# Kernel optimization log

Hardware: AMD Instinct MI355X
Metric: run time of the kernel (lower is better)

Reference implementation:

```python
import jax, jax.numpy as jnp
import numpy as np
from jax import lax

PATCH = 11          # patch_size
DIL = 2             # dilation_patch
PAD = (PATCH // 2) * DIL  # 10
EPS = 1e-5


def setup_inputs() -> dict:
    key = jax.random.key(0)
    k0, k1, kw, kb, kg, kbe = jax.random.split(key, 6)
    B, C, H, W = 8, 128, 192, 192
    x0 = jax.random.normal(k0, (B, C, H, W), dtype=jnp.float32)
    x1 = jax.random.normal(k1, (B, C, H, W), dtype=jnp.float32)
    # Conv2d(121, 8, k=3, s=1, p=1) params + BatchNorm2d(8) affine params
    conv_w = jax.random.normal(kw, (8, 121, 3, 3), dtype=jnp.float32) * 0.05
    conv_b = jax.random.normal(kb, (8,), dtype=jnp.float32) * 0.05
    gamma = jnp.ones((8,), dtype=jnp.float32)
    beta = jnp.zeros((8,), dtype=jnp.float32)
    return {"x0": x0, "x1": x1, "conv_w": conv_w, "conv_b": conv_b,
            "gamma": gamma, "beta": beta}


def _correlation(x0, x1):
    """spatial_correlation_sample(kernel=1, patch=11, stride=1, pad=0, dil_patch=2).
    out[b, pi*11+pj, i, j] = sum_c x0[b,c,i,j] * x1[b,c, i+(pi-5)*2, j+(pj-5)*2]
    (zero-padded outside)."""
    x1p = jnp.pad(x1, ((0, 0), (0, 0), (PAD, PAD), (PAD, PAD)))
    slices = []
    for pi in range(PATCH):       # static 11x11 displacement grid
        for pj in range(PATCH):
            x1s = lax.dynamic_slice(x1p, (0, 0, pi * DIL, pj * DIL), x1.shape)
            slices.append(jnp.einsum('bchw,bchw->bhw', x0, x1s))
    return jnp.stack(slices, axis=1)  # [B, 121, H, W]


def reference(x0, x1, conv_w, conv_b, gamma, beta):
    y = _correlation(x0, x1)  # [B, 121, H, W]
    y = lax.conv_general_dilated(y, conv_w, window_strides=(1, 1),
                                 padding=((1, 1), (1, 1)),
                                 dimension_numbers=('NCHW', 'OIHW', 'NCHW'))
    y = y + conv_b[None, :, None, None]
    # BatchNorm2d in training mode: batch statistics over (B, H, W), biased var
    mean = jnp.mean(y, axis=(0, 2, 3))
    var = jnp.var(y, axis=(0, 2, 3))
    y = (y - mean[None, :, None, None]) * (gamma / jnp.sqrt(var + EPS))[None, :, None, None] \
        + beta[None, :, None, None]
    return jax.nn.relu(y)
```

## Files before the change

kernel.cpp:

```cpp
#include <hip/hip_runtime.h>

#define HH 192
#define WW 192
#define CC 128
#define BB 8
#define HW (HH * WW)
#define OC 8
#define NPIX (BB * HW)
#define YCHUNK (OC * BB * HW)
#define X0ROW 24576
#define X1ROW 28672

typedef __attribute__((ext_vector_type(8))) short bf16x8;
typedef __attribute__((ext_vector_type(4))) float f32x4;

__device__ __forceinline__ unsigned short f2bf(float f) {
    unsigned int u = __float_as_uint(f);
    u += 0x7fffu + ((u >> 16) & 1u);
    return (unsigned short)(u >> 16);
}
__device__ __forceinline__ float bf2f(unsigned short u) {
    return __uint_as_float(((unsigned int)u) << 16);
}

__global__ __launch_bounds__(256) void k_pack(
    const float* __restrict__ x0, const float* __restrict__ x1,
    unsigned short* __restrict__ x0t, unsigned short* __restrict__ x1t)
{
    const int h = blockIdx.x, b = blockIdx.y, t = blockIdx.z;
    const float* src = t ? x1 : x0;
    __shared__ unsigned short lds[WW * 130];

    for (int idx = threadIdx.x; idx < CC * WW; idx += 256) {
        const int w = idx % WW, c = idx / WW;
        lds[w * 130 + c] = f2bf(src[((size_t)(b * CC + c) * HH + h) * WW + w]);
    }
    __syncthreads();

    if (t == 0) {
        uint4* dst = (uint4*)(x0t + (size_t)(b * HH + h) * X0ROW);
        for (int f8 = threadIdx.x; f8 < X0ROW / 8; f8 += 256) {
            const int pxl = f8 & 15;
            const int kg  = (f8 >> 4) & 3;
            const int q   = (f8 >> 6) & 3;
            const int pu  = f8 >> 8;
            const int ut  = pu % 6, par = pu / 6;
            const int px  = 2 * (16 * ut + pxl) + par;
            const unsigned short* s0 = &lds[px * 130 + q * 32 + kg * 8];
            uint4 v;
            v.x = s0[0] | ((unsigned int)s0[1] << 16);
            v.y = s0[2] | ((unsigned int)s0[3] << 16);
            v.z = s0[4] | ((unsigned int)s0[5] << 16);
            v.w = s0[6] | ((unsigned int)s0[7] << 16);
            dst[f8] = v;
        }
    } else {
        uint4* dst = (uint4*)(x1t + (size_t)(b * HH + h) * X1ROW);
        for (int f8 = threadIdx.x; f8 < X1ROW / 8; f8 += 256) {
            const int pxl = f8 & 15;
            const int kg  = (f8 >> 4) & 3;
            const int q   = (f8 >> 6) & 3;
            const int pv  = f8 >> 8;
            const int vt  = pv % 7, par = pv / 7;
            const int v   = 16 * vt - 8 + pxl;
            uint4 val = {0u, 0u, 0u, 0u};
            if (v >= 0 && v < 96) {
                const int px = 2 * v + par;
                const unsigned short* s0 = &lds[px * 130 + q * 32 + kg * 8];
                val.x = s0[0] | ((unsigned int)s0[1] << 16);
                val.y = s0[2] | ((unsigned int)s0[3] << 16);
                val.z = s0[4] | ((unsigned int)s0[5] << 16);
                val.w = s0[6] | ((unsigned int)s0[7] << 16);
            }
            dst[f8] = val;
        }
    }
}

__global__ __launch_bounds__(384, 8) void k_corr_mfma_conv(
    const unsigned short* __restrict__ x0t, const unsigned short* __restrict__ x1t,
    const float* __restrict__ cw, const float* __restrict__ cb,
    float* __restrict__ y0, float* __restrict__ y1,
    float* __restrict__ y2, float* __restrict__ y3, int split)
{
    const int L = blockIdx.x;
    const int N = 256 * split;
    const int w = (L & 7) * (N >> 3) + (L >> 3);
    const int G = 32 * split;
    const int b     = w / G;
    const int rem   = w % G;
    const int part  = rem >> 5;
    const int strip = rem & 31;
    const int i0    = strip * 6;
    const int plo   = (11 * part) / split;
    const int phi   = (11 * (part + 1)) / split;

    const int tid  = threadIdx.x;
    const int wave = tid >> 6, lane = tid & 63;
    const int ln15 = lane & 15, kg = lane >> 4;

    __shared__ unsigned short corr[8][194][11];

    if (tid < 176) {
        const int ir = tid / 22, rr = tid % 22;
        const int pj = rr % 11, jj = (rr < 11) ? 0 : 193;
        corr[ir][jj][pj] = 0;
    }

    float yacc[3][OC];
#pragma unroll
    for (int k = 0; k < 3; ++k)
#pragma unroll
        for (int o = 0; o < OC; ++o) yacc[k][o] = 0.f;

    const int jt  = tid % 192;
    const int irb = tid / 192;

    const unsigned short* x0b = x0t + (size_t)b * HH * X0ROW;
    const unsigned short* x1b = x1t + (size_t)b * HH * X1ROW;

    for (int pi = plo; pi < phi; ++pi) {
        __syncthreads();

        for (int g = wave; g < 96; g += 6) {
            const int ir  = g / 12, rr = g % 12;
            const int par = rr / 6, ut = rr % 6;
            const int u0  = ut * 16;
            const int i   = i0 - 1 + ir;
            const int r   = i + 2 * pi - 10;
            const bool gv = (i >= 0) && (i < HH) && (r >= 0) && (r < HH);
            const int icl = min(max(i, 0), HH - 1);
            const int rcl = min(max(r, 0), HH - 1);

            const unsigned short* pa =
                x0b + (size_t)icl * X0ROW + (par * 6 + ut) * 2048 + lane * 8;
            const bf16x8 a0 = *(const bf16x8*)(pa);
            const bf16x8 a1 = *(const bf16x8*)(pa + 512);
            const bf16x8 a2 = *(const bf16x8*)(pa + 1024);
            const bf16x8 a3 = *(const bf16x8*)(pa + 1536);

#pragma unroll
            for (int vtl = 0; vtl < 2; ++vtl) {
                const unsigned short* pb =
                    x1b + (size_t)rcl * X1ROW + (par * 7 + ut + vtl) * 2048 + lane * 8;
                const bf16x8 b0 = *(const bf16x8*)(pb);
                const bf16x8 b1 = *(const bf16x8*)(pb + 512);
                const bf16x8 b2 = *(const bf16x8*)(pb + 1024);
                const bf16x8 b3 = *(const bf16x8*)(pb + 1536);

                f32x4 c = {0.f, 0.f, 0.f, 0.f};
                c = __builtin_amdgcn_mfma_f32_16x16x32_bf16(a0, b0, c, 0, 0, 0);
                c = __builtin_amdgcn_mfma_f32_16x16x32_bf16(a1, b1, c, 0, 0, 0);
                c = __builtin_amdgcn_mfma_f32_16x16x32_bf16(a2, b2, c, 0, 0, 0);
                c = __builtin_amdgcn_mfma_f32_16x16x32_bf16(a3, b3, c, 0, 0, 0);

                const int v = u0 - 8 + 16 * vtl + ln15;
#pragma unroll
                for (int rg = 0; rg < 4; ++rg) {
                    const int u  = u0 + kg * 4 + rg;
                    const int pj = v - u + 5;
                    if (pj >= 0 && pj < 11)
                        corr[ir][2 * u + par + 1][pj] = f2bf(gv ? c[rg] : 0.f);
                }
            }
        }
        __syncthreads();

        for (int ki = 0; ki < 3; ++ki) {
            for (int kj = 0; kj < 3; ++kj) {
                float cv[3][11];
#pragma unroll
                for (int k = 0; k < 3; ++k) {
                    const unsigned short* cp = &corr[irb + 2 * k + ki][jt + kj][0];
#pragma unroll
                    for (int pj = 0; pj < 11; ++pj) cv[k][pj] = bf2f(cp[pj]);
                }
#pragma unroll
                for (int o = 0; o < OC; ++o) {
                    float a0 = yacc[0][o], a1 = yacc[1][o], a2 = yacc[2][o];
#pragma unroll
                    for (int pj = 0; pj < 11; ++pj) {
                        const float wv =
                            cw[o * 1089 + (pi * 11 + pj) * 9 + ki * 3 + kj];
                        a0 = fmaf(wv, cv[0][pj], a0);
                        a1 = fmaf(wv, cv[1][pj], a1);
                        a2 = fmaf(wv, cv[2][pj], a2);
                    }
                    yacc[0][o] = a0; yacc[1][o] = a1; yacc[2][o] = a2;
                }
            }
        }
    }

    float* yp = (part == 0) ? y0 : ((part == 1) ? y1 : ((part == 2) ? y2 : y3));
#pragma unroll
    for (int k = 0; k < 3; ++k) {
        const int irow = i0 + irb + 2 * k;
#pragma unroll
        for (int o = 0; o < OC; ++o) {
            float val = yacc[k][o];
            if (part == 0) val += cb[o];
            yp[((size_t)(b * OC + o) * HH + irow) * WW + jt] = val;
        }
    }
}

__global__ __launch_bounds__(256) void k_corr_conv(
    const float* __restrict__ x0, const float* __restrict__ x1,
    const float* __restrict__ cw, const float* __restrict__ cb,
    float* __restrict__ y)
{
    const int b  = blockIdx.z;
    const int i0 = blockIdx.y * 14;
    const int j0 = blockIdx.x * 14;
    const int li = threadIdx.x >> 4;
    const int lj = threadIdx.x & 15;
    const int gi = i0 + li - 1;
    const int gj = j0 + lj - 1;
    const bool valid    = (gi >= 0) & (gi < HH) & (gj >= 0) & (gj < WW);
    const bool interior = (li >= 1) & (li <= 14) & (lj >= 1) & (lj <= 14)
                        & (gi < HH) & (gj < WW);

    __shared__ float corr[16][16][13];

    float yacc[OC];
#pragma unroll
    for (int o = 0; o < OC; ++o) yacc[o] = 0.f;

    const size_t bbase = (size_t)b * CC * HW;
    const float* x0p = x0 + bbase + (size_t)gi * WW + gj;

    for (int pi = 0; pi < 11; ++pi) {
        float acc[11];
#pragma unroll
        for (int k = 0; k < 11; ++k) acc[k] = 0.f;

        const int r = gi + 2 * pi - 10;
        if (valid && r >= 0 && r < HH) {
            const float* p0 = x0p;
            if (gj >= 10 && gj <= WW - 11) {
                const float* p1o = x1 + bbase + (size_t)r * WW + (gj - 10);
#pragma unroll 2
                for (int c = 0; c < CC; ++c) {
                    const float a = *p0;
#pragma unroll
                    for (int k = 0; k < 11; ++k)
                        acc[k] = fmaf(a, p1o[2 * k], acc[k]);
                    p0 += HW; p1o += HW;
                }
            } else {
                const float* p1 = x1 + bbase + (size_t)r * WW;
#pragma unroll 2
                for (int c = 0; c < CC; ++c) {
                    const float a = *p0;
#pragma unroll
                    for (int k = 0; k < 11; ++k) {
                        const int col = gj + 2 * k - 10;
                        const float v = (col >= 0 && col < WW) ? p1[col] : 0.f;
                        acc[k] = fmaf(a, v, acc[k]);
                    }
                    p0 += HW; p1 += HW;
                }
            }
        }

        __syncthreads();
#pragma unroll
        for (int k = 0; k < 11; ++k) corr[li][lj][k] = acc[k];
        __syncthreads();

        if (interior) {
#pragma unroll
            for (int ki = 0; ki < 3; ++ki) {
#pragma unroll
                for (int kj = 0; kj < 3; ++kj) {
                    float cv[11];
#pragma unroll
                    for (int k = 0; k < 11; ++k)
                        cv[k] = corr[li + ki - 1][lj + kj - 1][k];
#pragma unroll
                    for (int o = 0; o < OC; ++o) {
#pragma unroll
                        for (int k = 0; k < 11; ++k) {
                            const float wv =
                                cw[(((o * 121) + pi * 11 + k) * 3 + ki) * 3 + kj];
                            yacc[o] = fmaf(wv, cv[k], yacc[o]);
                        }
                    }
                }
            }
        }
    }

    if (interior) {
#pragma unroll
        for (int o = 0; o < OC; ++o)
            y[(size_t)(b * OC + o) * HW + (size_t)gi * WW + gj] = yacc[o] + cb[o];
    }
}

__global__ __launch_bounds__(256) void k_stats_partial(
    const float* __restrict__ y0, const float* __restrict__ y1,
    const float* __restrict__ y2, const float* __restrict__ y3,
    int n, float* __restrict__ st)
{
    const int bid = blockIdx.x;
    const int b = bid >> 5, rem = bid & 31;
    const int o = rem >> 2, q = rem & 3;
    const size_t off = (size_t)(b * OC + o) * (HW / 4) + q * (HW / 16);
    const float4* p0 = (const float4*)y0 + off;
    const float4* p1 = (const float4*)y1 + off;
    const float4* p2 = (const float4*)y2 + off;
    const float4* p3 = (const float4*)y3 + off;
    float s = 0.f, qq = 0.f;
    for (int t = threadIdx.x; t < HW / 16; t += 256) {
        float4 z = p0[t];
        if (n >= 2) {
            const float4 v = p1[t];
            z.x += v.x; z.y += v.y; z.z += v.z; z.w += v.w;
        }
        if (n >= 3) {
            const float4 v = p2[t];
            z.x += v.x; z.y += v.y; z.z += v.z; z.w += v.w;
        }
        if (n >= 4) {
            const float4 v = p3[t];
            z.x += v.x; z.y += v.y; z.z += v.z; z.w += v.w;
        }
        s += z.x + z.y + z.z + z.w;
        qq = fmaf(z.x, z.x, qq); qq = fmaf(z.y, z.y, qq);
        qq = fmaf(z.z, z.z, qq); qq = fmaf(z.w, z.w, qq);
    }
#pragma unroll
    for (int off2 = 32; off2 > 0; off2 >>= 1) {
        s  += __shfl_down(s, off2);
        qq += __shfl_down(qq, off2);
    }
    __shared__ float ss[4], sq[4];
    const int lane = threadIdx.x & 63, wv = threadIdx.x >> 6;
    if (lane == 0) { ss[wv] = s; sq[wv] = qq; }
    __syncthreads();
    if (threadIdx.x == 0) {
        st[bid]       = ss[0] + ss[1] + ss[2] + ss[3];
        st[256 + bid] = sq[0] + sq[1] + sq[2] + sq[3];
    }
}

__global__ void k_stats_final(float* __restrict__ st,
                              const float* __restrict__ gamma,
                              const float* __restrict__ beta)
{
    const int o = threadIdx.x;
    if (o < 8) {
        float S = 0.f, Q = 0.f;
#pragma unroll
        for (int b = 0; b < 8; ++b)
#pragma unroll
            for (int q = 0; q < 4; ++q) {
                S += st[b * 32 + o * 4 + q];
                Q += st[256 + b * 32 + o * 4 + q];
            }
        const float invN = 1.f / (float)NPIX;
        const float mean = S * invN;
        const float var  = Q * invN - mean * mean;
        const float sc   = gamma[o] / sqrtf(var + 1e-5f);
        st[512 + o] = sc;
        st[520 + o] = beta[o] - mean * sc;
    }
}

__global__ __launch_bounds__(256) void k_bn_relu(
    const float* __restrict__ y0, const float* __restrict__ y1,
    const float* __restrict__ y2, const float* __restrict__ y3,
    int n, const float* __restrict__ st, float* __restrict__ out)
{
    const int i = blockIdx.x * 256 + threadIdx.x;
    const int o = (i / (HW / 4)) & 7;
    const float sc = st[512 + o], sh = st[520 + o];
    float4 z = ((const float4*)y0)[i];
    if (n >= 2) {
        const float4 v = ((const float4*)y1)[i];
        z.x += v.x; z.y += v.y; z.z += v.z; z.w += v.w;
    }
    if (n >= 3) {
        const float4 v = ((const float4*)y2)[i];
        z.x += v.x; z.y += v.y; z.z += v.z; z.w += v.w;
    }
    if (n >= 4) {
        const float4 v = ((const float4*)y3)[i];
        z.x += v.x; z.y += v.y; z.z += v.z; z.w += v.w;
    }
    float4 r;
    r.x = fmaxf(fmaf(z.x, sc, sh), 0.f);
    r.y = fmaxf(fmaf(z.y, sc, sh), 0.f);
    r.z = fmaxf(fmaf(z.z, sc, sh), 0.f);
    r.w = fmaxf(fmaf(z.w, sc, sh), 0.f);
    ((float4*)out)[i] = r;
}

extern "C" void kernel_launch(void* const* d_in, const int* in_sizes, int n_in,
                              void* d_out, int out_size, void* d_ws, size_t ws_size,
                              hipStream_t stream)
{
    const float* x0    = (const float*)d_in[0];
    const float* x1    = (const float*)d_in[1];
    const float* cw    = (const float*)d_in[2];
    const float* cb    = (const float*)d_in[3];
    const float* gamma = (const float*)d_in[4];
    const float* beta  = (const float*)d_in[5];
    float* out = (float*)d_out;
    float* st  = (float*)d_ws;

    const size_t x0bytes = (size_t)BB * HH * X0ROW * sizeof(unsigned short);
    const size_t x1bytes = (size_t)BB * HH * X1ROW * sizeof(unsigned short);
    const size_t ybytes  = (size_t)YCHUNK * sizeof(float);

    if (ws_size >= x0bytes + x1bytes + 2 * ybytes) {
        const int split = (ws_size >= x0bytes + x1bytes + 3 * ybytes) ? 4 : 3;

        unsigned short* x0t = (unsigned short*)d_ws;
        unsigned short* x1t = (unsigned short*)((char*)d_ws + x0bytes);
        float* y1 = (float*)((char*)d_ws + x0bytes + x1bytes);
        float* y2 = y1 + YCHUNK;
        float* y3 = (split == 4) ? (y2 + YCHUNK) : y2;

        k_pack<<<dim3(HH, BB, 2), 256, 0, stream>>>(x0, x1, x0t, x1t);
        k_corr_mfma_conv<<<256 * split, 384, 0, stream>>>(x0t, x1t, cw, cb,
                                                          out, y1, y2, y3, split);
        k_stats_partial<<<256, 256, 0, stream>>>(out, y1, y2, y3, split, st);
        k_stats_final<<<1, 64, 0, stream>>>(st, gamma, beta);
        k_bn_relu<<<(YCHUNK / 4) / 256, 256, 0, stream>>>(out, y1, y2, y3,
                                                          split, st, out);
    } else {
        dim3 g1(14, 14, 8);
        k_corr_conv<<<g1, 256, 0, stream>>>(x0, x1, cw, cb, out);
        k_stats_partial<<<64 * 4, 256, 0, stream>>>(out, out, out, out, 1, st);
        k_stats_final<<<1, 64, 0, stream>>>(st, gamma, beta);
        k_bn_relu<<<(YCHUNK / 4) / 256, 256, 0, stream>>>(out, out, out, out,
                                                          1, st, out);
    }
}
```

Before: 566.1 us.

## Fix displacement split at three and fold partial sums in stats pass

```diff
diff --git a/kernel.cpp b/kernel.cpp
--- a/kernel.cpp
+++ b/kernel.cpp
@@ -80,20 +80,17 @@
 __global__ __launch_bounds__(384, 8) void k_corr_mfma_conv(
     const unsigned short* __restrict__ x0t, const unsigned short* __restrict__ x1t,
     const float* __restrict__ cw, const float* __restrict__ cb,
-    float* __restrict__ y0, float* __restrict__ y1,
-    float* __restrict__ y2, float* __restrict__ y3, int split)
+    float* __restrict__ y0, float* __restrict__ y1, float* __restrict__ y2)
 {
     const int L = blockIdx.x;
-    const int N = 256 * split;
-    const int w = (L & 7) * (N >> 3) + (L >> 3);
-    const int G = 32 * split;
-    const int b     = w / G;
-    const int rem   = w % G;
+    const int w = (L & 7) * 96 + (L >> 3);
+    const int b     = w / 96;
+    const int rem   = w % 96;
     const int part  = rem >> 5;
     const int strip = rem & 31;
     const int i0    = strip * 6;
-    const int plo   = (11 * part) / split;
-    const int phi   = (11 * (part + 1)) / split;
+    const int plo   = (11 * part) / 3;
+    const int phi   = (11 * (part + 1)) / 3;
 
     const int tid  = threadIdx.x;
     const int wave = tid >> 6, lane = tid & 63;
@@ -192,7 +189,7 @@
         }
     }
 
-    float* yp = (part == 0) ? y0 : ((part == 1) ? y1 : ((part == 2) ? y2 : y3));
+    float* yp = (part == 0) ? y0 : ((part == 1) ? y1 : y2);
 #pragma unroll
     for (int k = 0; k < 3; ++k) {
         const int irow = i0 + irb + 2 * k;
@@ -300,18 +297,16 @@
 }
 
 __global__ __launch_bounds__(256) void k_stats_partial(
-    const float* __restrict__ y0, const float* __restrict__ y1,
-    const float* __restrict__ y2, const float* __restrict__ y3,
-    int n, float* __restrict__ st)
+    float* __restrict__ y0, const float* __restrict__ y1,
+    const float* __restrict__ y2, int n, float* __restrict__ st)
 {
     const int bid = blockIdx.x;
     const int b = bid >> 5, rem = bid & 31;
     const int o = rem >> 2, q = rem & 3;
     const size_t off = (size_t)(b * OC + o) * (HW / 4) + q * (HW / 16);
-    const float4* p0 = (const float4*)y0 + off;
+    float4* p0       = (float4*)y0 + off;
     const float4* p1 = (const float4*)y1 + off;
     const float4* p2 = (const float4*)y2 + off;
-    const float4* p3 = (const float4*)y3 + off;
     float s = 0.f, qq = 0.f;
     for (int t = threadIdx.x; t < HW / 16; t += 256) {
         float4 z = p0[t];
@@ -323,10 +318,7 @@
             const float4 v = p2[t];
             z.x += v.x; z.y += v.y; z.z += v.z; z.w += v.w;
         }
-        if (n >= 4) {
-            const float4 v = p3[t];
-            z.x += v.x; z.y += v.y; z.z += v.z; z.w += v.w;
-        }
+        if (n >= 2) p0[t] = z;
         s += z.x + z.y + z.z + z.w;
         qq = fmaf(z.x, z.x, qq); qq = fmaf(z.y, z.y, qq);
         qq = fmaf(z.z, z.z, qq); qq = fmaf(z.w, z.w, qq);
@@ -370,32 +362,17 @@
 }
 
 __global__ __launch_bounds__(256) void k_bn_relu(
-    const float* __restrict__ y0, const float* __restrict__ y1,
-    const float* __restrict__ y2, const float* __restrict__ y3,
-    int n, const float* __restrict__ st, float* __restrict__ out)
+    float* __restrict__ y, const float* __restrict__ st)
 {
     const int i = blockIdx.x * 256 + threadIdx.x;
     const int o = (i / (HW / 4)) & 7;
     const float sc = st[512 + o], sh = st[520 + o];
-    float4 z = ((const float4*)y0)[i];
-    if (n >= 2) {
-        const float4 v = ((const float4*)y1)[i];
-        z.x += v.x; z.y += v.y; z.z += v.z; z.w += v.w;
-    }
-    if (n >= 3) {
-        const float4 v = ((const float4*)y2)[i];
-        z.x += v.x; z.y += v.y; z.z += v.z; z.w += v.w;
-    }
-    if (n >= 4) {
-        const float4 v = ((const float4*)y3)[i];
-        z.x += v.x; z.y += v.y; z.z += v.z; z.w += v.w;
-    }
-    float4 r;
-    r.x = fmaxf(fmaf(z.x, sc, sh), 0.f);
-    r.y = fmaxf(fmaf(z.y, sc, sh), 0.f);
-    r.z = fmaxf(fmaf(z.z, sc, sh), 0.f);
-    r.w = fmaxf(fmaf(z.w, sc, sh), 0.f);
-    ((float4*)out)[i] = r;
+    float4 v = ((float4*)y)[i];
+    v.x = fmaxf(fmaf(v.x, sc, sh), 0.f);
+    v.y = fmaxf(fmaf(v.y, sc, sh), 0.f);
+    v.z = fmaxf(fmaf(v.z, sc, sh), 0.f);
+    v.w = fmaxf(fmaf(v.w, sc, sh), 0.f);
+    ((float4*)y)[i] = v;
 }
 
 extern "C" void kernel_launch(void* const* d_in, const int* in_sizes, int n_in,
@@ -416,27 +393,21 @@
     const size_t ybytes  = (size_t)YCHUNK * sizeof(float);
 
     if (ws_size >= x0bytes + x1bytes + 2 * ybytes) {
-        const int split = (ws_size >= x0bytes + x1bytes + 3 * ybytes) ? 4 : 3;
-
         unsigned short* x0t = (unsigned short*)d_ws;
         unsigned short* x1t = (unsigned short*)((char*)d_ws + x0bytes);
         float* y1 = (float*)((char*)d_ws + x0bytes + x1bytes);
         float* y2 = y1 + YCHUNK;
-        float* y3 = (split == 4) ? (y2 + YCHUNK) : y2;
 
         k_pack<<<dim3(HH, BB, 2), 256, 0, stream>>>(x0, x1, x0t, x1t);
-        k_corr_mfma_conv<<<256 * split, 384, 0, stream>>>(x0t, x1t, cw, cb,
-                                                          out, y1, y2, y3, split);
-        k_stats_partial<<<256, 256, 0, stream>>>(out, y1, y2, y3, split, st);
+        k_corr_mfma_conv<<<768, 384, 0, stream>>>(x0t, x1t, cw, cb, out, y1, y2);
+        k_stats_partial<<<256, 256, 0, stream>>>(out, y1, y2, 3, st);
         k_stats_final<<<1, 64, 0, stream>>>(st, gamma, beta);
-        k_bn_relu<<<(YCHUNK / 4) / 256, 256, 0, stream>>>(out, y1, y2, y3,
-                                                          split, st, out);
+        k_bn_relu<<<(YCHUNK / 4) / 256, 256, 0, stream>>>(out, st);
     } else {
         dim3 g1(14, 14, 8);
         k_corr_conv<<<g1, 256, 0, stream>>>(x0, x1, cw, cb, out);
-        k_stats_partial<<<64 * 4, 256, 0, stream>>>(out, out, out, out, 1, st);
+        k_stats_partial<<<256, 256, 0, stream>>>(out, out, out, 1, st);
         k_stats_final<<<1, 64, 0, stream>>>(st, gamma, beta);
-        k_bn_relu<<<(YCHUNK / 4) / 256, 256, 0, stream>>>(out, out, out, out,
-                                                          1, st, out);
-    }
-}
+        k_bn_relu<<<(YCHUNK / 4) / 256, 256, 0, stream>>>(out, st);
+    }
+}
```

Result: faster. 522.2 us (-7.7%).
